# Kernel optimization log

Hardware: AMD Instinct MI355X
Metric: run time of the kernel (lower is better)

## Reference

```python
import jax, jax.numpy as jnp
import numpy as np

V, D, DK, H, HID, NB = 8192, 768, 64, 12, 3072, 4
B, S = 4, 1024


def setup_inputs() -> dict:
    key = jax.random.key(0)
    ks = jax.random.split(key, 10)
    def n(k, shape):
        return jax.random.normal(k, shape, jnp.float32) * 0.02
    return dict(
        X=jax.random.uniform(ks[0], (B, S, V), jnp.float32),
        emb_w=n(ks[1], (V, D)), emb_b=jnp.zeros((D,), jnp.float32),
        Wq=n(ks[2], (NB, H, D, DK)), bq=jnp.zeros((NB, H, DK), jnp.float32),
        Wk=n(ks[3], (NB, H, D, DK)), bk=jnp.zeros((NB, H, DK), jnp.float32),
        Wv=n(ks[4], (NB, H, D, DK)), bv=jnp.zeros((NB, H, DK), jnp.float32),
        Wo=n(ks[5], (NB, H * DK, D)), bo=jnp.zeros((NB, D), jnp.float32),
        W1=n(ks[6], (NB, D, HID)), b1=jnp.zeros((NB, HID), jnp.float32),
        W2=n(ks[7], (NB, HID, D)), b2=jnp.zeros((NB, D), jnp.float32),
        Wout=n(ks[8], (D, V)), bout=jnp.zeros((V,), jnp.float32),
    )


def layernorm(X):
    # custom LayerNorm: no eps, no affine, population variance over dim 2
    mu = jnp.mean(X, axis=2, keepdims=True)
    sigma = jnp.sqrt(jnp.mean(jnp.square(X - mu), axis=2, keepdims=True))
    return (X - mu) / sigma


def reference(X, emb_w, emb_b, Wq, bq, Wk, bk, Wv, bv, Wo, bo, W1, b1, W2, b2, Wout, bout):
    b, s, _ = X.shape
    sqrt_dk = jnp.sqrt(jnp.float32(DK))
    causal = jnp.tril(jnp.ones((s, s), bool))  # tril applied to scores BEFORE softmax (zeros, not -inf) — faithful
    X = X @ emb_w + emb_b  # [b,s,d]
    for i in range(NB):
        Q = jnp.einsum('bsd,hde->bhse', X, Wq[i]) + bq[i][None, :, None, :]
        K = jnp.einsum('bsd,hde->bhse', X, Wk[i]) + bk[i][None, :, None, :]
        Vv = jnp.einsum('bsd,hde->bhse', X, Wv[i]) + bv[i][None, :, None, :]
        scores = jnp.einsum('bhqe,bhke->bhqk', Q, K)
        scores = jnp.where(causal, scores, 0.0) / sqrt_dk
        A = jax.nn.softmax(scores, axis=-1)
        # original einsum 'ijk,ijl->ijl': sum attention weights over k, scale V
        head_out = jnp.sum(A, axis=-1, keepdims=True) * Vv  # [b,h,s,dk]
        cat = head_out.transpose(0, 2, 1, 3).reshape(b, s, H * DK)
        O = cat @ Wo[i] + bo[i]
        X = layernorm(X + O)
        F = jax.nn.relu(X @ W1[i] + b1[i]) @ W2[i] + b2[i]
        X = layernorm(X + F)
    return jax.nn.softmax(X @ Wout + bout, axis=2)
```

## Files before the change

kernel.cpp:

```cpp
#include <hip/hip_runtime.h>

typedef __bf16 bf16_t;
typedef __bf16 bf16x4 __attribute__((ext_vector_type(4)));
typedef __bf16 bf16x8 __attribute__((ext_vector_type(8)));
typedef float f32x4 __attribute__((ext_vector_type(4)));

#define BM 128
#define BN 128
#define BK 32
#define LDK 40

__device__ inline uint4 pack_bf16x8(float4 a, float4 b)
{
    union { bf16_t h[8]; uint4 u; } cv;
    cv.h[0] = (bf16_t)a.x; cv.h[1] = (bf16_t)a.y;
    cv.h[2] = (bf16_t)a.z; cv.h[3] = (bf16_t)a.w;
    cv.h[4] = (bf16_t)b.x; cv.h[5] = (bf16_t)b.y;
    cv.h[6] = (bf16_t)b.z; cv.h[7] = (bf16_t)b.w;
    return cv.u;
}

template<bool AF32>
__global__ __launch_bounds__(256, 2)
void gemm_bf16(const bf16_t* __restrict__ A, const float* __restrict__ Af,
               const bf16_t* __restrict__ Bt, const float* __restrict__ bias,
               float* __restrict__ Cf, bf16_t* __restrict__ Cbf,
               int M, int N, int K, int relu, int kChunk, long zStride)
{
    __shared__ bf16_t As[BM * LDK];
    __shared__ bf16_t Bs[BN * LDK];

    const int gx = gridDim.x, gy = gridDim.y;
    const long L = blockIdx.x + (long)gx * (blockIdx.y + (long)gy * blockIdx.z);
    const int  r = (int)(L & 7);
    const long t = L >> 3;
    const int  bx = (int)(t % gx);
    const long g  = r + 8 * (t / gx);
    const int  by = (int)(g % gy);
    const int  bz = (int)(g / gy);

    const int tid  = threadIdx.x;
    const int m0   = by * BM;
    const int n0   = bx * BN;
    const int z    = bz;
    const int wave = tid >> 6;
    const int lane = tid & 63;
    const int wm   = (wave & 1) * 64;
    const int wn   = (wave >> 1) * 64;
    const int lr   = lane & 15;
    const int lq   = lane >> 4;

    int kBeg = 0, kEnd = K;
    const float* biasP = bias;
    if (kChunk > 0) {
        kBeg = z * kChunk;
        kEnd = min(K, kBeg + kChunk);
        if (Cbf) Cbf += (long)z * M * N;
        else     Cf  += (long)z * M * N;
        if (z != 0) biasP = nullptr;
    } else if (zStride != 0) {
        if constexpr (AF32) Af += (long)z * zStride;
        else                A  += (long)z * zStride;
        Bt += (long)z * zStride;
        if (Cf)  Cf  += (long)z * zStride;
        if (Cbf) Cbf += (long)z * zStride;
    }

    f32x4 acc[4][4];
#pragma unroll
    for (int i = 0; i < 4; i++)
#pragma unroll
        for (int j = 0; j < 4; j++) acc[i][j] = (f32x4){0.f, 0.f, 0.f, 0.f};

    const int c0 = tid, c1 = tid + 256;
    const int ar0 = c0 >> 2, ak0 = (c0 & 3) * 8;
    const int ar1 = c1 >> 2, ak1 = (c1 & 3) * 8;

    const bf16_t* Bptr = Bt + (long)n0 * K;

    for (int k0 = kBeg; k0 < kEnd; k0 += BK) {
        uint4 av0, av1;
        if constexpr (AF32) {
            const float* p0 = Af + (long)(m0 + ar0) * K + k0 + ak0;
            const float* p1 = Af + (long)(m0 + ar1) * K + k0 + ak1;
            float4 a00 = *(const float4*)p0, a01 = *(const float4*)(p0 + 4);
            float4 a10 = *(const float4*)p1, a11 = *(const float4*)(p1 + 4);
            av0 = pack_bf16x8(a00, a01);
            av1 = pack_bf16x8(a10, a11);
        } else {
            av0 = *(const uint4*)(A + (long)(m0 + ar0) * K + k0 + ak0);
            av1 = *(const uint4*)(A + (long)(m0 + ar1) * K + k0 + ak1);
        }
        uint4 bv0 = *(const uint4*)(Bptr + (long)ar0 * K + k0 + ak0);
        uint4 bv1 = *(const uint4*)(Bptr + (long)ar1 * K + k0 + ak1);
        __syncthreads();
        *(uint4*)&As[ar0 * LDK + ak0] = av0;
        *(uint4*)&As[ar1 * LDK + ak1] = av1;
        *(uint4*)&Bs[ar0 * LDK + ak0] = bv0;
        *(uint4*)&Bs[ar1 * LDK + ak1] = bv1;
        __syncthreads();

        bf16x8 af[4], bfr[4];
#pragma unroll
        for (int i = 0; i < 4; i++) {
            af[i]  = *(bf16x8*)&As[(wm + i * 16 + lr) * LDK + lq * 8];
            bfr[i] = *(bf16x8*)&Bs[(wn + i * 16 + lr) * LDK + lq * 8];
        }
#pragma unroll
        for (int i = 0; i < 4; i++)
#pragma unroll
            for (int j = 0; j < 4; j++)
                acc[i][j] = __builtin_amdgcn_mfma_f32_16x16x32_bf16(
                    af[i], bfr[j], acc[i][j], 0, 0, 0);
    }

#pragma unroll
    for (int i = 0; i < 4; i++) {
#pragma unroll
        for (int j = 0; j < 4; j++) {
            const int col = n0 + wn + j * 16 + lr;
            const float bval = biasP ? biasP[col] : 0.f;
#pragma unroll
            for (int rr = 0; rr < 4; rr++) {
                const int row = m0 + wm + i * 16 + lq * 4 + rr;
                float v = acc[i][j][rr] + bval;
                if (relu) v = fmaxf(v, 0.f);
                const long idx = (long)row * N + col;
                if (Cf)  Cf[idx] = v;
                if (Cbf) Cbf[idx] = (bf16_t)v;
            }
        }
    }
}

__global__ void transpose_cast(const float* __restrict__ in, bf16_t* __restrict__ out,
                               int R, int C, long inStrideZ, long outStrideZ)
{
    __shared__ float t[32][33];
    const float* inz = in + inStrideZ * blockIdx.z;
    bf16_t* outz = out + outStrideZ * blockIdx.z;
    const int c0 = blockIdx.x * 32;
    const int r0 = blockIdx.y * 32;
    const int tx = threadIdx.x, ty = threadIdx.y;
#pragma unroll
    for (int dy = 0; dy < 32; dy += 8)
        t[ty + dy][tx] = inz[(long)(r0 + ty + dy) * C + c0 + tx];
    __syncthreads();
#pragma unroll
    for (int dy = 0; dy < 32; dy += 8)
        outz[(long)(c0 + ty + dy) * R + r0 + tx] = (bf16_t)t[tx][ty + dy];
}

__global__ void build_wvn(const float* __restrict__ Wv, bf16_t* __restrict__ WvN)
{
    const long o = (long)blockIdx.x * 256 + threadIdx.x;
    const int e = (int)(o & 63);
    const int h = (int)((o >> 6) % 12);
    const long t = o / 768;
    const int d = (int)(t % 768);
    const int i = (int)(t / 768);
    WvN[o] = (bf16_t)Wv[(((long)(i * 12 + h) * 768 + d) << 6) + e];
}

__global__ __launch_bounds__(256)
void build_bvo(const float* __restrict__ Wo, const float* __restrict__ bv,
               const float* __restrict__ bo, float* __restrict__ bvo)
{
    const int i = blockIdx.y;
    const int j = blockIdx.x * 256 + threadIdx.x;
    const float* w = Wo + (long)i * 589824 + j;
    const float* b = bv + i * 768;
    float s = bo[i * 768 + j];
    for (int n = 0; n < 768; n++) s += b[n] * w[(long)n * 768];
    bvo[i * 768 + j] = s;
}

__global__ __launch_bounds__(256)
void reduce_cast(const bf16_t* __restrict__ P, long pStride, int nP,
                 float* __restrict__ outF, bf16_t* __restrict__ outBf, long n)
{
    const long i = ((long)blockIdx.x * 256 + threadIdx.x) * 8;
    if (i + 8 > n) return;
    float s[8] = {0.f, 0.f, 0.f, 0.f, 0.f, 0.f, 0.f, 0.f};
    for (int p = 0; p < nP; p++) {
        bf16x8 v = *(const bf16x8*)(P + (long)p * pStride + i);
#pragma unroll
        for (int e = 0; e < 8; e++) s[e] += (float)v[e];
    }
    *(float4*)(outF + i)     = (float4){s[0], s[1], s[2], s[3]};
    *(float4*)(outF + i + 4) = (float4){s[4], s[5], s[6], s[7]};
    union { bf16_t h[8]; uint4 u; } cv;
#pragma unroll
    for (int e = 0; e < 8; e++) cv.h[e] = (bf16_t)s[e];
    *(uint4*)(outBf + i) = cv.u;
}

__global__ __launch_bounds__(192)
void ln_residual(float* __restrict__ X, const bf16_t* __restrict__ P,
                 long pStride, int nP, bf16_t* __restrict__ Xbf)
{
    __shared__ float red[8];
    const long base = (long)blockIdx.x * 768;
    const int tid = threadIdx.x;
    const int i0 = tid * 4;
    float4 xv = *(const float4*)(X + base + i0);
    float s[4] = {xv.x, xv.y, xv.z, xv.w};
    for (int p = 0; p < nP; p++) {
        bf16x4 pv = *(const bf16x4*)(P + (long)p * pStride + base + i0);
        s[0] += (float)pv[0]; s[1] += (float)pv[1];
        s[2] += (float)pv[2]; s[3] += (float)pv[3];
    }
    float sum = s[0] + s[1] + s[2] + s[3];
    for (int o = 32; o > 0; o >>= 1) sum += __shfl_down(sum, o, 64);
    if ((tid & 63) == 0) red[tid >> 6] = sum;
    __syncthreads();
    const float mu = (red[0] + red[1] + red[2]) * (1.0f / 768.0f);
    float d0 = s[0] - mu, d1 = s[1] - mu, d2 = s[2] - mu, d3 = s[3] - mu;
    float sq = d0 * d0 + d1 * d1 + d2 * d2 + d3 * d3;
    for (int o = 32; o > 0; o >>= 1) sq += __shfl_down(sq, o, 64);
    if ((tid & 63) == 0) red[4 + (tid >> 6)] = sq;
    __syncthreads();
    const float var = (red[4] + red[5] + red[6]) * (1.0f / 768.0f);
    const float rstd = 1.0f / sqrtf(var);
    union { bf16_t h[4]; uint2 u; } cv;
#pragma unroll
    for (int j = 0; j < 4; j++) {
        const float v = (s[j] - mu) * rstd;
        X[base + i0 + j] = v;
        cv.h[j] = (bf16_t)v;
    }
    *(uint2*)(Xbf + base + i0) = cv.u;
}

__global__ __launch_bounds__(256)
void softmax_bf16(const bf16_t* __restrict__ L, float* __restrict__ out)
{
    __shared__ float red[8];
    const long base = (long)blockIdx.x * 8192;
    const int tid = threadIdx.x;
    float v[32];
    float mx = -1e30f;
#pragma unroll
    for (int gq = 0; gq < 4; gq++) {
        bf16x8 h = *(const bf16x8*)(L + base + gq * 2048 + tid * 8);
#pragma unroll
        for (int e = 0; e < 8; e++) {
            v[gq * 8 + e] = (float)h[e];
            mx = fmaxf(mx, v[gq * 8 + e]);
        }
    }
    for (int o = 32; o > 0; o >>= 1) mx = fmaxf(mx, __shfl_down(mx, o, 64));
    if ((tid & 63) == 0) red[tid >> 6] = mx;
    __syncthreads();
    mx = fmaxf(fmaxf(red[0], red[1]), fmaxf(red[2], red[3]));
    float sum = 0.f;
#pragma unroll
    for (int j = 0; j < 32; j++) {
        v[j] = __expf(v[j] - mx);
        sum += v[j];
    }
    for (int o = 32; o > 0; o >>= 1) sum += __shfl_down(sum, o, 64);
    if ((tid & 63) == 0) red[4 + (tid >> 6)] = sum;
    __syncthreads();
    const float inv = 1.0f / (red[4] + red[5] + red[6] + red[7]);
#pragma unroll
    for (int gq = 0; gq < 4; gq++) {
        const long o0 = base + gq * 2048 + tid * 8;
        *(float4*)(out + o0) = (float4){v[gq*8+0]*inv, v[gq*8+1]*inv,
                                        v[gq*8+2]*inv, v[gq*8+3]*inv};
        *(float4*)(out + o0 + 4) = (float4){v[gq*8+4]*inv, v[gq*8+5]*inv,
                                            v[gq*8+6]*inv, v[gq*8+7]*inv};
    }
}

extern "C" void kernel_launch(void* const* d_in, const int* in_sizes, int n_in,
                              void* d_out, int out_size, void* d_ws, size_t ws_size,
                              hipStream_t stream)
{
    (void)in_sizes; (void)n_in; (void)out_size; (void)ws_size;
    const float* X0   = (const float*)d_in[0];
    const float* embw = (const float*)d_in[1];
    const float* embb = (const float*)d_in[2];
    const float* Wv   = (const float*)d_in[7];
    const float* bv   = (const float*)d_in[8];
    const float* Wo   = (const float*)d_in[9];
    const float* bo   = (const float*)d_in[10];
    const float* W1   = (const float*)d_in[11];
    const float* b1   = (const float*)d_in[12];
    const float* W2   = (const float*)d_in[13];
    const float* b2   = (const float*)d_in[14];
    const float* Wout = (const float*)d_in[15];
    const float* bout = (const float*)d_in[16];
    float* out = (float*)d_out;

    char* base = (char*)d_ws;
    bf16_t* P     = (bf16_t*)base;
    bf16_t* WvN   = (bf16_t*)base;
    bf16_t* WoT   = (bf16_t*)(base + 4718592);
    bf16_t* Lbf   = (bf16_t*)base;
    bf16_t* Hid   = (bf16_t*)(base + 50331648);
    bf16_t* embT  = (bf16_t*)(base + 75497472);
    bf16_t* WoutT = (bf16_t*)(base + 75497472);
    bf16_t* WvoT  = (bf16_t*)(base + 88080384);
    float*  bvo   = (float*)(base + 92798976);
    bf16_t* W1T   = (bf16_t*)(base + 92811264);
    bf16_t* W2T   = (bf16_t*)(base + 111685632);
    float*  Xf    = (float*)(base + 130560000);
    bf16_t* Xbf   = (bf16_t*)(base + 143142912);

    const dim3 tb(32, 8);
    const long MN = 3145728;

    transpose_cast<<<dim3(24, 256, 1), tb, 0, stream>>>(embw, embT, 8192, 768, 0, 0);
    transpose_cast<<<dim3(24, 24, 4), tb, 0, stream>>>(Wo, WoT, 768, 768, 589824, 589824);
    build_wvn<<<9216, 256, 0, stream>>>(Wv, WvN);
    build_bvo<<<dim3(3, 4), 256, 0, stream>>>(Wo, bv, bo, bvo);
    gemm_bf16<false><<<dim3(6, 6, 4), 256, 0, stream>>>(
        WoT, nullptr, WvN, nullptr, nullptr, WvoT, 768, 768, 768, 0, 0, 589824L);
    transpose_cast<<<dim3(96, 24, 4), tb, 0, stream>>>(W1, W1T, 768, 3072, 2359296, 2359296);
    transpose_cast<<<dim3(24, 96, 4), tb, 0, stream>>>(W2, W2T, 3072, 768, 2359296, 2359296);

    gemm_bf16<true><<<dim3(6, 32, 8), 256, 0, stream>>>(
        nullptr, X0, embT, embb, nullptr, P, 4096, 768, 8192, 0, 1024, 0);
    reduce_cast<<<1536, 256, 0, stream>>>(P, MN, 8, Xf, Xbf, MN);

    for (int i = 0; i < 4; i++) {
        gemm_bf16<false><<<dim3(6, 32, 4), 256, 0, stream>>>(
            Xbf, nullptr, WvoT + (size_t)i * 589824, bvo + i * 768, nullptr, P,
            4096, 768, 768, 0, 192, 0);
        ln_residual<<<4096, 192, 0, stream>>>(Xf, P, MN, 4, Xbf);
        gemm_bf16<false><<<dim3(24, 32), 256, 0, stream>>>(
            Xbf, nullptr, W1T + (size_t)i * 2359296, b1 + i * 3072, nullptr, Hid,
            4096, 3072, 768, 1, 0, 0);
        gemm_bf16<false><<<dim3(6, 32, 4), 256, 0, stream>>>(
            Hid, nullptr, W2T + (size_t)i * 2359296, b2 + i * 768, nullptr, P,
            4096, 768, 3072, 0, 768, 0);
        ln_residual<<<4096, 192, 0, stream>>>(Xf, P, MN, 4, Xbf);
    }

    transpose_cast<<<dim3(256, 24, 1), tb, 0, stream>>>(Wout, WoutT, 768, 8192, 0, 0);
    gemm_bf16<false><<<dim3(64, 32), 256, 0, stream>>>(
        Xbf, nullptr, WoutT, bout, nullptr, Lbf, 4096, 8192, 768, 0, 0, 0);
    softmax_bf16<<<4096, 256, 0, stream>>>(Lbf, out);
}
```

Measured before the change: 1.087 ms.

## Double-buffer GEMM with direct global-to-LDS loads and pre-cast embedding input

```diff
diff --git a/kernel.cpp b/kernel.cpp
--- a/kernel.cpp
+++ b/kernel.cpp
@@ -8,41 +8,35 @@
 #define BM 128
 #define BN 128
 #define BK 32
-#define LDK 40
-
-__device__ inline uint4 pack_bf16x8(float4 a, float4 b)
-{
-    union { bf16_t h[8]; uint4 u; } cv;
-    cv.h[0] = (bf16_t)a.x; cv.h[1] = (bf16_t)a.y;
-    cv.h[2] = (bf16_t)a.z; cv.h[3] = (bf16_t)a.w;
-    cv.h[4] = (bf16_t)b.x; cv.h[5] = (bf16_t)b.y;
-    cv.h[6] = (bf16_t)b.z; cv.h[7] = (bf16_t)b.w;
-    return cv.u;
-}
-
-template<bool AF32>
-__global__ __launch_bounds__(256, 2)
-void gemm_bf16(const bf16_t* __restrict__ A, const float* __restrict__ Af,
-               const bf16_t* __restrict__ Bt, const float* __restrict__ bias,
+
+__device__ __forceinline__ void gload16(const bf16_t* g, bf16_t* l)
+{
+    __builtin_amdgcn_global_load_lds(
+        (const __attribute__((address_space(1))) void*)g,
+        (__attribute__((address_space(3))) void*)l, 16, 0, 0);
+}
+
+__global__ __launch_bounds__(256, 3)
+void gemm_bf16(const bf16_t* __restrict__ A, const bf16_t* __restrict__ Bt,
+               const float* __restrict__ bias,
                float* __restrict__ Cf, bf16_t* __restrict__ Cbf,
                int M, int N, int K, int relu, int kChunk, long zStride)
 {
-    __shared__ bf16_t As[BM * LDK];
-    __shared__ bf16_t Bs[BN * LDK];
+    __shared__ __align__(16) bf16_t As[2][BM * BK];
+    __shared__ __align__(16) bf16_t Bs[2][BN * BK];
 
     const int gx = gridDim.x, gy = gridDim.y;
-    const long L = blockIdx.x + (long)gx * (blockIdx.y + (long)gy * blockIdx.z);
-    const int  r = (int)(L & 7);
-    const long t = L >> 3;
-    const int  bx = (int)(t % gx);
-    const long g  = r + 8 * (t / gx);
-    const int  by = (int)(g % gy);
-    const int  bz = (int)(g / gy);
+    const long Lb = blockIdx.x + (long)gx * (blockIdx.y + (long)gy * blockIdx.z);
+    const int  rb = (int)(Lb & 7);
+    const long tbk = Lb >> 3;
+    const int  bx = (int)(tbk % gx);
+    const long gb = rb + 8 * (tbk / gx);
+    const int  by = (int)(gb % gy);
+    const int  bz = (int)(gb / gy);
 
     const int tid  = threadIdx.x;
     const int m0   = by * BM;
     const int n0   = bx * BN;
-    const int z    = bz;
     const int wave = tid >> 6;
     const int lane = tid & 63;
     const int wm   = (wave & 1) * 64;
@@ -53,17 +47,16 @@
     int kBeg = 0, kEnd = K;
     const float* biasP = bias;
     if (kChunk > 0) {
-        kBeg = z * kChunk;
+        kBeg = bz * kChunk;
         kEnd = min(K, kBeg + kChunk);
-        if (Cbf) Cbf += (long)z * M * N;
-        else     Cf  += (long)z * M * N;
-        if (z != 0) biasP = nullptr;
+        if (Cbf) Cbf += (long)bz * M * N;
+        else     Cf  += (long)bz * M * N;
+        if (bz != 0) biasP = nullptr;
     } else if (zStride != 0) {
-        if constexpr (AF32) Af += (long)z * zStride;
-        else                A  += (long)z * zStride;
-        Bt += (long)z * zStride;
-        if (Cf)  Cf  += (long)z * zStride;
-        if (Cbf) Cbf += (long)z * zStride;
+        A  += (long)bz * zStride;
+        Bt += (long)bz * zStride;
+        if (Cf)  Cf  += (long)bz * zStride;
+        if (Cbf) Cbf += (long)bz * zStride;
     }
 
     f32x4 acc[4][4];
@@ -72,39 +65,38 @@
 #pragma unroll
         for (int j = 0; j < 4; j++) acc[i][j] = (f32x4){0.f, 0.f, 0.f, 0.f};
 
-    const int c0 = tid, c1 = tid + 256;
-    const int ar0 = c0 >> 2, ak0 = (c0 & 3) * 8;
-    const int ar1 = c1 >> 2, ak1 = (c1 & 3) * 8;
-
-    const bf16_t* Bptr = Bt + (long)n0 * K;
-
-    for (int k0 = kBeg; k0 < kEnd; k0 += BK) {
-        uint4 av0, av1;
-        if constexpr (AF32) {
-            const float* p0 = Af + (long)(m0 + ar0) * K + k0 + ak0;
-            const float* p1 = Af + (long)(m0 + ar1) * K + k0 + ak1;
-            float4 a00 = *(const float4*)p0, a01 = *(const float4*)(p0 + 4);
-            float4 a10 = *(const float4*)p1, a11 = *(const float4*)(p1 + 4);
-            av0 = pack_bf16x8(a00, a01);
-            av1 = pack_bf16x8(a10, a11);
-        } else {
-            av0 = *(const uint4*)(A + (long)(m0 + ar0) * K + k0 + ak0);
-            av1 = *(const uint4*)(A + (long)(m0 + ar1) * K + k0 + ak1);
+    const int c0  = wave * 128 + lane;
+    const int c1  = c0 + 64;
+    const int sw0 = ((c0 & 3) ^ ((c0 >> 3) & 3)) * 8;
+    const int sw1 = ((c1 & 3) ^ ((c1 >> 3) & 3)) * 8;
+    const bf16_t* gA0 = A  + (long)(m0 + (c0 >> 2)) * K + kBeg + sw0;
+    const bf16_t* gA1 = A  + (long)(m0 + (c1 >> 2)) * K + kBeg + sw1;
+    const bf16_t* gB0 = Bt + (long)(n0 + (c0 >> 2)) * K + kBeg + sw0;
+    const bf16_t* gB1 = Bt + (long)(n0 + (c1 >> 2)) * K + kBeg + sw1;
+    const int lb0 = wave * 1024;
+    const int lb1 = wave * 1024 + 512;
+    const int lqx8 = (lq ^ ((lr >> 1) & 3)) * 8;
+
+    const int nt = (kEnd - kBeg) / BK;
+
+    gload16(gA0, &As[0][lb0]); gload16(gA1, &As[0][lb1]);
+    gload16(gB0, &Bs[0][lb0]); gload16(gB1, &Bs[0][lb1]);
+    __syncthreads();
+
+    long ko = BK;
+    int cur = 0;
+    for (int t = 0; t < nt; ++t) {
+        if (t + 1 < nt) {
+            const int nx = cur ^ 1;
+            gload16(gA0 + ko, &As[nx][lb0]); gload16(gA1 + ko, &As[nx][lb1]);
+            gload16(gB0 + ko, &Bs[nx][lb0]); gload16(gB1 + ko, &Bs[nx][lb1]);
+            ko += BK;
         }
-        uint4 bv0 = *(const uint4*)(Bptr + (long)ar0 * K + k0 + ak0);
-        uint4 bv1 = *(const uint4*)(Bptr + (long)ar1 * K + k0 + ak1);
-        __syncthreads();
-        *(uint4*)&As[ar0 * LDK + ak0] = av0;
-        *(uint4*)&As[ar1 * LDK + ak1] = av1;
-        *(uint4*)&Bs[ar0 * LDK + ak0] = bv0;
-        *(uint4*)&Bs[ar1 * LDK + ak1] = bv1;
-        __syncthreads();
-
         bf16x8 af[4], bfr[4];
 #pragma unroll
         for (int i = 0; i < 4; i++) {
-            af[i]  = *(bf16x8*)&As[(wm + i * 16 + lr) * LDK + lq * 8];
-            bfr[i] = *(bf16x8*)&Bs[(wn + i * 16 + lr) * LDK + lq * 8];
+            af[i]  = *(const bf16x8*)&As[cur][(wm + i * 16 + lr) * BK + lqx8];
+            bfr[i] = *(const bf16x8*)&Bs[cur][(wn + i * 16 + lr) * BK + lqx8];
         }
 #pragma unroll
         for (int i = 0; i < 4; i++)
@@ -112,6 +104,8 @@
             for (int j = 0; j < 4; j++)
                 acc[i][j] = __builtin_amdgcn_mfma_f32_16x16x32_bf16(
                     af[i], bfr[j], acc[i][j], 0, 0, 0);
+        __syncthreads();
+        cur ^= 1;
     }
 
 #pragma unroll
@@ -131,6 +125,21 @@
             }
         }
     }
+}
+
+__global__ __launch_bounds__(256)
+void cast_bf16(const float* __restrict__ in, bf16_t* __restrict__ out, long n)
+{
+    long i = ((long)blockIdx.x * blockDim.x + threadIdx.x) * 8;
+    if (i + 8 > n) return;
+    float4 f0 = *(const float4*)(in + i);
+    float4 f1 = *(const float4*)(in + i + 4);
+    union { bf16_t h[8]; uint4 u; } cv;
+    cv.h[0] = (bf16_t)f0.x; cv.h[1] = (bf16_t)f0.y;
+    cv.h[2] = (bf16_t)f0.z; cv.h[3] = (bf16_t)f0.w;
+    cv.h[4] = (bf16_t)f1.x; cv.h[5] = (bf16_t)f1.y;
+    cv.h[6] = (bf16_t)f1.z; cv.h[7] = (bf16_t)f1.w;
+    *(uint4*)(out + i) = cv.u;
 }
 
 __global__ void transpose_cast(const float* __restrict__ in, bf16_t* __restrict__ out,
@@ -294,52 +303,55 @@
     float* out = (float*)d_out;
 
     char* base = (char*)d_ws;
-    bf16_t* P     = (bf16_t*)base;
-    bf16_t* WvN   = (bf16_t*)base;
-    bf16_t* WoT   = (bf16_t*)(base + 4718592);
+    bf16_t* X0bf  = (bf16_t*)base;
+    float*  Xf    = (float*)base;
+    bf16_t* W1T   = (bf16_t*)(base + 12582912);
+    bf16_t* W2T   = (bf16_t*)(base + 31457280);
     bf16_t* Lbf   = (bf16_t*)base;
-    bf16_t* Hid   = (bf16_t*)(base + 50331648);
-    bf16_t* embT  = (bf16_t*)(base + 75497472);
-    bf16_t* WoutT = (bf16_t*)(base + 75497472);
-    bf16_t* WvoT  = (bf16_t*)(base + 88080384);
-    float*  bvo   = (float*)(base + 92798976);
-    bf16_t* W1T   = (bf16_t*)(base + 92811264);
-    bf16_t* W2T   = (bf16_t*)(base + 111685632);
-    float*  Xf    = (float*)(base + 130560000);
-    bf16_t* Xbf   = (bf16_t*)(base + 143142912);
+    bf16_t* P     = (bf16_t*)(base + 67108864);
+    bf16_t* WvN   = (bf16_t*)(base + 67108864);
+    bf16_t* WoT   = (bf16_t*)(base + 71827456);
+    bf16_t* Hid   = (bf16_t*)(base + 92274688);
+    bf16_t* embT  = (bf16_t*)(base + 117440512);
+    bf16_t* WoutT = (bf16_t*)(base + 117440512);
+    bf16_t* WvoT  = (bf16_t*)(base + 130023424);
+    float*  bvo   = (float*)(base + 134742016);
+    bf16_t* Xbf   = (bf16_t*)(base + 134754304);
 
     const dim3 tb(32, 8);
     const long MN = 3145728;
 
+    cast_bf16<<<16384, 256, 0, stream>>>(X0, X0bf, (long)33554432);
     transpose_cast<<<dim3(24, 256, 1), tb, 0, stream>>>(embw, embT, 8192, 768, 0, 0);
     transpose_cast<<<dim3(24, 24, 4), tb, 0, stream>>>(Wo, WoT, 768, 768, 589824, 589824);
     build_wvn<<<9216, 256, 0, stream>>>(Wv, WvN);
     build_bvo<<<dim3(3, 4), 256, 0, stream>>>(Wo, bv, bo, bvo);
-    gemm_bf16<false><<<dim3(6, 6, 4), 256, 0, stream>>>(
-        WoT, nullptr, WvN, nullptr, nullptr, WvoT, 768, 768, 768, 0, 0, 589824L);
+    gemm_bf16<<<dim3(6, 6, 4), 256, 0, stream>>>(
+        WoT, WvN, nullptr, nullptr, WvoT, 768, 768, 768, 0, 0, 589824L);
+
+    gemm_bf16<<<dim3(6, 32, 4), 256, 0, stream>>>(
+        X0bf, embT, embb, nullptr, P, 4096, 768, 8192, 0, 2048, 0);
+    reduce_cast<<<1536, 256, 0, stream>>>(P, MN, 4, Xf, Xbf, MN);
+
     transpose_cast<<<dim3(96, 24, 4), tb, 0, stream>>>(W1, W1T, 768, 3072, 2359296, 2359296);
     transpose_cast<<<dim3(24, 96, 4), tb, 0, stream>>>(W2, W2T, 3072, 768, 2359296, 2359296);
 
-    gemm_bf16<true><<<dim3(6, 32, 8), 256, 0, stream>>>(
-        nullptr, X0, embT, embb, nullptr, P, 4096, 768, 8192, 0, 1024, 0);
-    reduce_cast<<<1536, 256, 0, stream>>>(P, MN, 8, Xf, Xbf, MN);
-
     for (int i = 0; i < 4; i++) {
-        gemm_bf16<false><<<dim3(6, 32, 4), 256, 0, stream>>>(
-            Xbf, nullptr, WvoT + (size_t)i * 589824, bvo + i * 768, nullptr, P,
+        gemm_bf16<<<dim3(6, 32, 4), 256, 0, stream>>>(
+            Xbf, WvoT + (size_t)i * 589824, bvo + i * 768, nullptr, P,
             4096, 768, 768, 0, 192, 0);
         ln_residual<<<4096, 192, 0, stream>>>(Xf, P, MN, 4, Xbf);
-        gemm_bf16<false><<<dim3(24, 32), 256, 0, stream>>>(
-            Xbf, nullptr, W1T + (size_t)i * 2359296, b1 + i * 3072, nullptr, Hid,
+        gemm_bf16<<<dim3(24, 32), 256, 0, stream>>>(
+            Xbf, W1T + (size_t)i * 2359296, b1 + i * 3072, nullptr, Hid,
             4096, 3072, 768, 1, 0, 0);
-        gemm_bf16<false><<<dim3(6, 32, 4), 256, 0, stream>>>(
-            Hid, nullptr, W2T + (size_t)i * 2359296, b2 + i * 768, nullptr, P,
+        gemm_bf16<<<dim3(6, 32, 4), 256, 0, stream>>>(
+            Hid, W2T + (size_t)i * 2359296, b2 + i * 768, nullptr, P,
             4096, 768, 3072, 0, 768, 0);
         ln_residual<<<4096, 192, 0, stream>>>(Xf, P, MN, 4, Xbf);
     }
 
     transpose_cast<<<dim3(256, 24, 1), tb, 0, stream>>>(Wout, WoutT, 768, 8192, 0, 0);
-    gemm_bf16<false><<<dim3(64, 32), 256, 0, stream>>>(
-        Xbf, nullptr, WoutT, bout, nullptr, Lbf, 4096, 8192, 768, 0, 0, 0);
+    gemm_bf16<<<dim3(64, 32), 256, 0, stream>>>(
+        Xbf, WoutT, bout, nullptr, Lbf, 4096, 8192, 768, 0, 0, 0);
     softmax_bf16<<<4096, 256, 0, stream>>>(Lbf, out);
 }
```

New measurement: 1.008 ms. 7.2% less time.
